# Kernel optimization log

Measured on AMD Instinct MI355X. Metric: run time of the kernel, lower is better.

Reference implementation:

```python
import jax, jax.numpy as jnp
import numpy as np

B, N, C = 4, 2048, 512
H = 8
HD = C // H  # 64
SCALE = HD ** -0.5


def setup_inputs() -> dict:
    key = jax.random.key(0)
    k1, k2, k3 = jax.random.split(key, 3)
    x = jax.random.normal(k1, (B, N, C), dtype=jnp.float32)
    w_qkv = jax.random.normal(k2, (3 * C, C), dtype=jnp.float32) * (C ** -0.5)
    b_qkv = jnp.zeros((3 * C,), dtype=jnp.float32)
    w_proj = jax.random.normal(k3, (C, C), dtype=jnp.float32) * (C ** -0.5)
    b_proj = jnp.zeros((C,), dtype=jnp.float32)
    return {"x": x, "w_qkv": w_qkv, "b_qkv": b_qkv, "w_proj": w_proj, "b_proj": b_proj}


def reference(x, w_qkv, b_qkv, w_proj, b_proj):
    # qkv projection: (B,N,C) @ (C,3C) -> (B,N,3,H,HD) -> (3,B,H,N,HD)
    qkv = (x @ w_qkv.T + b_qkv).reshape(B, N, 3, H, HD).transpose(2, 0, 3, 1, 4)
    q, k, v = qkv[0], qkv[1], qkv[2]
    # scores (B,H,N,N), scale applied after matmul as in the torch source
    attn = jnp.einsum('bhnd,bhmd->bhnm', q, k) * SCALE
    attn = jax.nn.softmax(attn, axis=-1)
    out = jnp.einsum('bhnm,bhmd->bhnd', attn, v)  # (B,H,N,HD)
    out = out.transpose(0, 2, 1, 3).reshape(B, N, C)
    return out @ w_proj.T + b_proj
```

## Files before the change

### kernel.cpp

```cpp
#include <hip/hip_runtime.h>

#define B_ 4
#define N_ 2048
#define C_ 512
#define H_ 8
#define HD_ 64
#define SCALE_ 0.125f
#define QSCALE_ 0.18033688011112042f

typedef __attribute__((ext_vector_type(8))) __bf16 bf16x8;
typedef __attribute__((ext_vector_type(4))) float f32x4;
typedef __attribute__((ext_vector_type(4))) unsigned int u32x4;
typedef __attribute__((ext_vector_type(2))) unsigned int u32x2;
typedef __attribute__((ext_vector_type(4))) short s16x4;

#if __has_builtin(__builtin_amdgcn_mfma_f32_16x16x16bf16_1k)
#define MFMA16(acc, a, b) acc = __builtin_amdgcn_mfma_f32_16x16x16bf16_1k(a, b, acc, 0, 0, 0)
#else
#define MFMA16(acc, a, b) \
    asm("v_mfma_f32_16x16x16_bf16 %0, %1, %2, %0" : "+v"(acc) : "v"(a), "v"(b))
#endif

__device__ __forceinline__ unsigned short f2bf(float f) {
    unsigned int u = __builtin_bit_cast(unsigned int, f);
    u += 0x7fffu + ((u >> 16) & 1u);
    return (unsigned short)(u >> 16);
}

__device__ __forceinline__ void llds16(const void* g, void* l) {
    __builtin_amdgcn_global_load_lds(
        (const __attribute__((address_space(1))) unsigned int*)g,
        (__attribute__((address_space(3))) unsigned int*)l, 16, 0, 0);
}

__global__ __launch_bounds__(256) void cvt_all(const float* __restrict__ x,
                                               const float* __restrict__ wq,
                                               const float* __restrict__ wp,
                                               unsigned short* __restrict__ xb,
                                               unsigned short* __restrict__ wqb,
                                               unsigned short* __restrict__ wpb) {
    const int NX = B_ * N_ * C_ / 4, NQ = 3 * C_ * C_ / 4, NP = C_ * C_ / 4;
    int i = blockIdx.x * 256 + threadIdx.x;
    const float4* src;
    ushort4* dst;
    int idx;
    if (i < NX) { src = (const float4*)x; dst = (ushort4*)xb; idx = i; }
    else if (i < NX + NQ) { src = (const float4*)wq; dst = (ushort4*)wqb; idx = i - NX; }
    else if (i < NX + NQ + NP) { src = (const float4*)wp; dst = (ushort4*)wpb; idx = i - NX - NQ; }
    else return;
    float4 v = src[idx];
    ushort4 o;
    o.x = f2bf(v.x); o.y = f2bf(v.y); o.z = f2bf(v.z); o.w = f2bf(v.w);
    dst[idx] = o;
}

template <int MODE>
__global__ __launch_bounds__(256) void gemm_bt(const unsigned short* __restrict__ A,
                                               const unsigned short* __restrict__ Bw,
                                               const float* __restrict__ bias,
                                               float* __restrict__ Out,
                                               unsigned short* __restrict__ Qb,
                                               unsigned short* __restrict__ Kb,
                                               unsigned short* __restrict__ Vt) {
    constexpr int K = 512;
    __shared__ __align__(16) unsigned char smem[32768];
    unsigned char* sA = smem;
    unsigned char* sB = smem + 16384;

    const int tid = threadIdx.x;
    const int lane = tid & 63;
    const int wave = tid >> 6;
    const int wm = wave >> 1, wn = wave & 1;
    const int m0 = blockIdx.y * 128;
    const int n0 = blockIdx.x * 128;

    f32x4 acc[4][4] = {};

    for (int k0 = 0; k0 < K; k0 += 64) {
#pragma unroll
        for (int i = 0; i < 4; i++) {
            int ci = wave * 4 + i;
            int row = ci * 8 + (lane >> 3);
            int cb = (lane & 7) * 16;
            const unsigned char* ga =
                (const unsigned char*)A + ((size_t)(m0 + row) * K + k0) * 2 + cb;
            const unsigned char* gb =
                (const unsigned char*)Bw + ((size_t)(n0 + row) * K + k0) * 2 + cb;
            llds16(ga, sA + ci * 1024);
            llds16(gb, sB + ci * 1024);
        }
        __syncthreads();
#pragma unroll
        for (int kk = 0; kk < 2; kk++) {
            bf16x8 af[4], bfr[4];
#pragma unroll
            for (int mi = 0; mi < 4; mi++)
                af[mi] = *(const bf16x8*)(sA + (wm * 64 + mi * 16 + (lane & 15)) * 128 +
                                          kk * 64 + (lane >> 4) * 16);
#pragma unroll
            for (int ni = 0; ni < 4; ni++)
                bfr[ni] = *(const bf16x8*)(sB + (wn * 64 + ni * 16 + (lane & 15)) * 128 +
                                           kk * 64 + (lane >> 4) * 16);
#pragma unroll
            for (int mi = 0; mi < 4; mi++)
#pragma unroll
                for (int ni = 0; ni < 4; ni++)
                    acc[mi][ni] = __builtin_amdgcn_mfma_f32_16x16x32_bf16(
                        af[mi], bfr[ni], acc[mi][ni], 0, 0, 0);
        }
        __syncthreads();
    }

    if constexpr (MODE == 0) {
        if (n0 >= 1024) {
            unsigned char* T = smem;
#pragma unroll
            for (int ni = 0; ni < 4; ni++) {
                int cl = wn * 64 + ni * 16 + (lane & 15);
                float bv = bias[n0 + cl];
#pragma unroll
                for (int mi = 0; mi < 4; mi++) {
#pragma unroll
                    for (int r = 0; r < 4; r++) {
                        int ml = wm * 64 + mi * 16 + ((lane >> 4) << 2) + r;
                        *(unsigned short*)(T + cl * 256 + ((ml * 2) ^ ((cl & 7) << 4))) =
                            f2bf(acc[mi][ni][r] + bv);
                    }
                }
            }
            __syncthreads();
            const int b = m0 >> 11;
#pragma unroll
            for (int it = 0; it < 8; it++) {
                int li = it * 256 + tid;
                int cl2 = li >> 4, mc = li & 15;
                int cg = n0 + cl2;
                int h = (cg >> 6) & 7, d = cg & 63;
                u32x4 vv = *(const u32x4*)(T + cl2 * 256 + ((mc * 16) ^ ((cl2 & 7) << 4)));
                int n = (m0 & (N_ - 1)) + mc * 8;
                *(u32x4*)((unsigned char*)Vt +
                          (((size_t)(b * H_ + h) * HD_ + d) * N_ + n) * 2) = vv;
            }
        } else {
            const bool selq = (n0 < 512);
#pragma unroll
            for (int ni = 0; ni < 4; ni++) {
                int cg = n0 + wn * 64 + ni * 16 + (lane & 15);
                int h = (cg >> 6) & 7, d = cg & 63;
                float bv = bias[cg];
#pragma unroll
                for (int mi = 0; mi < 4; mi++) {
#pragma unroll
                    for (int r = 0; r < 4; r++) {
                        int m = m0 + wm * 64 + mi * 16 + ((lane >> 4) << 2) + r;
                        int b = m >> 11, n = m & (N_ - 1);
                        float fv = acc[mi][ni][r] + bv;
                        size_t idx = ((size_t)(b * H_ + h) * N_ + n) * HD_ + d;
                        if (selq) Qb[idx] = f2bf(fv * QSCALE_);
                        else Kb[idx] = f2bf(fv);
                    }
                }
            }
        }
    } else {
#pragma unroll
        for (int ni = 0; ni < 4; ni++) {
            int c = n0 + wn * 64 + ni * 16 + (lane & 15);
            float bv = bias[c];
#pragma unroll
            for (int mi = 0; mi < 4; mi++) {
#pragma unroll
                for (int r = 0; r < 4; r++) {
                    int m = m0 + wm * 64 + mi * 16 + ((lane >> 4) << 2) + r;
                    Out[(size_t)m * C_ + c] = acc[mi][ni][r] + bv;
                }
            }
        }
    }
}

__global__ __launch_bounds__(512, 4) void attn_fwd(const unsigned short* __restrict__ Qb,
                                                   const unsigned short* __restrict__ Kb,
                                                   const unsigned short* __restrict__ Vt,
                                                   unsigned short* __restrict__ AO) {
    __shared__ __align__(16) unsigned char smem[32768];

    const int tid = threadIdx.x, lane = tid & 63, wave = tid >> 6;
    const int g = lane >> 4, c = lane & 15;
    const int L = blockIdx.y * 16 + blockIdx.x;
    const int bh = (L & 7) * 4 + ((L >> 3) & 3);
    const int qx = L >> 5;
    const int q0 = qx * 128 + wave * 16;
    const unsigned short* Qh = Qb + (size_t)bh * N_ * HD_;
    const unsigned short* Kh = Kb + (size_t)bh * N_ * HD_;
    const unsigned short* Vh = Vt + (size_t)bh * HD_ * N_;

    bf16x8 qf[2];
#pragma unroll
    for (int kk = 0; kk < 2; kk++)
        qf[kk] = *(const bf16x8*)(Qh + (size_t)(q0 + c) * HD_ + kk * 32 + g * 8);

    s16x4 ones16;
#pragma unroll
    for (int i = 0; i < 4; i++) ones16[i] = (short)0x3F80;

    f32x4 o[4] = {};
    f32x4 osum = {};

    const int srow = tid >> 3;
    const int sslot = (tid & 7) * 16;
    const int ssw = (sslot ^ ((srow & 7) << 4));

    {
        u32x4 kreg = *(const u32x4*)((const unsigned char*)Kh + (size_t)srow * 128 + sslot);
        u32x4 vreg = *(const u32x4*)((const unsigned char*)Vh + (size_t)srow * (N_ * 2) + sslot);
        *(u32x4*)(smem + srow * 128 + ssw) = kreg;
        *(u32x4*)(smem + 16384 + srow * 128 + ssw) = vreg;
    }
    __syncthreads();

#pragma unroll 1
    for (int t = 0; t < N_ / 64; t++) {
        unsigned char* bK = smem + (t & 1) * 8192;
        unsigned char* bV = smem + 16384 + (t & 1) * 8192;

        u32x4 kreg, vreg;
        if (t < N_ / 64 - 1) {
            int kv0 = (t + 1) * 64;
            kreg = *(const u32x4*)((const unsigned char*)Kh + (size_t)(kv0 + srow) * 128 + sslot);
            vreg = *(const u32x4*)((const unsigned char*)Vh + (size_t)srow * (N_ * 2) +
                                   kv0 * 2 + sslot);
        }

        f32x4 s[4] = {};
#pragma unroll
        for (int j = 0; j < 4; j++) {
#pragma unroll
            for (int kk = 0; kk < 2; kk++) {
                int krow = j * 16 + c;
                bf16x8 kf = *(const bf16x8*)(bK + krow * 128 +
                                             ((kk * 64 + g * 16) ^ ((krow & 7) << 4)));
                s[j] = __builtin_amdgcn_mfma_f32_16x16x32_bf16(kf, qf[kk], s[j], 0, 0, 0);
            }
        }

        s16x4 pa[4];
#pragma unroll
        for (int j = 0; j < 4; j++) {
            float p0 = __builtin_exp2f(s[j][0]);
            float p1 = __builtin_exp2f(s[j][1]);
            float p2 = __builtin_exp2f(s[j][2]);
            float p3 = __builtin_exp2f(s[j][3]);
            unsigned int lo, hi;
            asm("v_cvt_pk_bf16_f32 %0, %1, %2" : "=v"(lo) : "v"(p0), "v"(p1));
            asm("v_cvt_pk_bf16_f32 %0, %1, %2" : "=v"(hi) : "v"(p2), "v"(p3));
            u32x2 w;
            w[0] = lo;
            w[1] = hi;
            pa[j] = __builtin_bit_cast(s16x4, w);
        }

#pragma unroll
        for (int j = 0; j < 4; j++) {
            MFMA16(osum, pa[j], ones16);
#pragma unroll
            for (int dj = 0; dj < 4; dj++) {
                int vrow = dj * 16 + c;
                u32x2 vv = *(const u32x2*)(bV + vrow * 128 +
                                           ((j * 32 + 8 * g) ^ ((vrow & 7) << 4)));
                s16x4 vfj = __builtin_bit_cast(s16x4, vv);
                MFMA16(o[dj], pa[j], vfj);
            }
        }

        if (t < N_ / 64 - 1) {
            unsigned char* nK = smem + ((t + 1) & 1) * 8192;
            unsigned char* nV = smem + 16384 + ((t + 1) & 1) * 8192;
            *(u32x4*)(nK + srow * 128 + ssw) = kreg;
            *(u32x4*)(nV + srow * 128 + ssw) = vreg;
        }
        __syncthreads();
    }

    const int b = bh >> 3, h = bh & 7;
#pragma unroll
    for (int r = 0; r < 4; r++) {
        float inv = 1.0f / osum[r];
        int n = q0 + (g << 2) + r;
#pragma unroll
        for (int dj = 0; dj < 4; dj++) {
            int col = h * HD_ + dj * 16 + c;
            AO[((size_t)(b * N_ + n)) * C_ + col] = f2bf(o[dj][r] * inv);
        }
    }
}

extern "C" void kernel_launch(void* const* d_in, const int* in_sizes, int n_in,
                              void* d_out, int out_size, void* d_ws, size_t ws_size,
                              hipStream_t stream) {
    const float* x = (const float*)d_in[0];
    const float* w_qkv = (const float*)d_in[1];
    const float* b_qkv = (const float*)d_in[2];
    const float* w_proj = (const float*)d_in[3];
    const float* b_proj = (const float*)d_in[4];
    float* out = (float*)d_out;

    unsigned char* ws = (unsigned char*)d_ws;
    unsigned short* xb = (unsigned short*)ws;
    unsigned short* AO = xb;
    unsigned short* wqb = (unsigned short*)(ws + 8388608);
    unsigned short* wpb = (unsigned short*)(ws + 8388608 + 1572864);
    unsigned short* Vt = (unsigned short*)(ws + 8388608 + 1572864 + 524288);

    unsigned short* Qb = (unsigned short*)d_out;
    unsigned short* Kb = Qb + (size_t)B_ * H_ * N_ * HD_;

    const int NALL = (B_ * N_ * C_ + 3 * C_ * C_ + C_ * C_) / 4;
    cvt_all<<<(NALL + 255) / 256, 256, 0, stream>>>(x, w_qkv, w_proj, xb, wqb, wpb);

    gemm_bt<0><<<dim3(12, 64), 256, 0, stream>>>(xb, wqb, b_qkv, nullptr, Qb, Kb, Vt);
    attn_fwd<<<dim3(16, 32), 512, 0, stream>>>(Qb, Kb, Vt, AO);
    gemm_bt<1><<<dim3(4, 64), 256, 0, stream>>>(AO, wpb, b_proj, out, nullptr, nullptr, nullptr);
}
```

Measured before the change: 112.1 us.

## Split attention waves across KV halves with 32-row query tiles and LDS reduction

Each wave now handles 32 query rows and half of each 64-key tile, instead of 16 query rows over the full tile. Each K and V fragment read from LDS feeds two MFMAs, so LDS reads per MFMA drop. The two key-half partial outputs and row sums are combined through shared memory at the end. This costs a larger LDS allocation, more accumulator registers and an extra barrier plus reduction in the epilogue.

```diff
diff --git a/kernel.cpp b/kernel.cpp
--- a/kernel.cpp
+++ b/kernel.cpp
@@ -183,29 +183,33 @@
                                                    const unsigned short* __restrict__ Kb,
                                                    const unsigned short* __restrict__ Vt,
                                                    unsigned short* __restrict__ AO) {
-    __shared__ __align__(16) unsigned char smem[32768];
+    __shared__ __align__(16) unsigned char smem[40960];
 
     const int tid = threadIdx.x, lane = tid & 63, wave = tid >> 6;
     const int g = lane >> 4, c = lane & 15;
+    const int wq = wave >> 1, wk = wave & 1;
     const int L = blockIdx.y * 16 + blockIdx.x;
     const int bh = (L & 7) * 4 + ((L >> 3) & 3);
     const int qx = L >> 5;
-    const int q0 = qx * 128 + wave * 16;
+    const int q0 = qx * 128 + wq * 32;
     const unsigned short* Qh = Qb + (size_t)bh * N_ * HD_;
     const unsigned short* Kh = Kb + (size_t)bh * N_ * HD_;
     const unsigned short* Vh = Vt + (size_t)bh * HD_ * N_;
 
-    bf16x8 qf[2];
-#pragma unroll
-    for (int kk = 0; kk < 2; kk++)
-        qf[kk] = *(const bf16x8*)(Qh + (size_t)(q0 + c) * HD_ + kk * 32 + g * 8);
+    bf16x8 qf[2][2];
+#pragma unroll
+    for (int u = 0; u < 2; u++)
+#pragma unroll
+        for (int kk = 0; kk < 2; kk++)
+            qf[u][kk] = *(const bf16x8*)(Qh + (size_t)(q0 + u * 16 + c) * HD_ +
+                                         kk * 32 + g * 8);
 
     s16x4 ones16;
 #pragma unroll
     for (int i = 0; i < 4; i++) ones16[i] = (short)0x3F80;
 
-    f32x4 o[4] = {};
-    f32x4 osum = {};
+    f32x4 o[2][4] = {};
+    f32x4 osum[2] = {};
 
     const int srow = tid >> 3;
     const int sslot = (tid & 7) * 16;
@@ -232,44 +236,49 @@
                                    kv0 * 2 + sslot);
         }
 
-        f32x4 s[4] = {};
-#pragma unroll
-        for (int j = 0; j < 4; j++) {
+        f32x4 s[2][2] = {};
+#pragma unroll
+        for (int j = 0; j < 2; j++) {
 #pragma unroll
             for (int kk = 0; kk < 2; kk++) {
-                int krow = j * 16 + c;
+                int krow = wk * 32 + j * 16 + c;
                 bf16x8 kf = *(const bf16x8*)(bK + krow * 128 +
                                              ((kk * 64 + g * 16) ^ ((krow & 7) << 4)));
-                s[j] = __builtin_amdgcn_mfma_f32_16x16x32_bf16(kf, qf[kk], s[j], 0, 0, 0);
-            }
-        }
-
-        s16x4 pa[4];
-#pragma unroll
-        for (int j = 0; j < 4; j++) {
-            float p0 = __builtin_exp2f(s[j][0]);
-            float p1 = __builtin_exp2f(s[j][1]);
-            float p2 = __builtin_exp2f(s[j][2]);
-            float p3 = __builtin_exp2f(s[j][3]);
-            unsigned int lo, hi;
-            asm("v_cvt_pk_bf16_f32 %0, %1, %2" : "=v"(lo) : "v"(p0), "v"(p1));
-            asm("v_cvt_pk_bf16_f32 %0, %1, %2" : "=v"(hi) : "v"(p2), "v"(p3));
-            u32x2 w;
-            w[0] = lo;
-            w[1] = hi;
-            pa[j] = __builtin_bit_cast(s16x4, w);
-        }
-
-#pragma unroll
-        for (int j = 0; j < 4; j++) {
-            MFMA16(osum, pa[j], ones16);
+                s[0][j] = __builtin_amdgcn_mfma_f32_16x16x32_bf16(kf, qf[0][kk], s[0][j], 0, 0, 0);
+                s[1][j] = __builtin_amdgcn_mfma_f32_16x16x32_bf16(kf, qf[1][kk], s[1][j], 0, 0, 0);
+            }
+        }
+
+        s16x4 pa[2][2];
+#pragma unroll
+        for (int u = 0; u < 2; u++)
+#pragma unroll
+            for (int j = 0; j < 2; j++) {
+                float p0 = __builtin_exp2f(s[u][j][0]);
+                float p1 = __builtin_exp2f(s[u][j][1]);
+                float p2 = __builtin_exp2f(s[u][j][2]);
+                float p3 = __builtin_exp2f(s[u][j][3]);
+                unsigned int lo, hi;
+                asm("v_cvt_pk_bf16_f32 %0, %1, %2" : "=v"(lo) : "v"(p0), "v"(p1));
+                asm("v_cvt_pk_bf16_f32 %0, %1, %2" : "=v"(hi) : "v"(p2), "v"(p3));
+                u32x2 w;
+                w[0] = lo;
+                w[1] = hi;
+                pa[u][j] = __builtin_bit_cast(s16x4, w);
+            }
+
+#pragma unroll
+        for (int j = 0; j < 2; j++) {
+            MFMA16(osum[0], pa[0][j], ones16);
+            MFMA16(osum[1], pa[1][j], ones16);
 #pragma unroll
             for (int dj = 0; dj < 4; dj++) {
                 int vrow = dj * 16 + c;
                 u32x2 vv = *(const u32x2*)(bV + vrow * 128 +
-                                           ((j * 32 + 8 * g) ^ ((vrow & 7) << 4)));
+                                           ((wk * 64 + j * 32 + 8 * g) ^ ((vrow & 7) << 4)));
                 s16x4 vfj = __builtin_bit_cast(s16x4, vv);
-                MFMA16(o[dj], pa[j], vfj);
+                MFMA16(o[0][dj], pa[0][j], vfj);
+                MFMA16(o[1][dj], pa[1][j], vfj);
             }
         }
 
@@ -282,16 +291,39 @@
         __syncthreads();
     }
 
-    const int b = bh >> 3, h = bh & 7;
-#pragma unroll
-    for (int r = 0; r < 4; r++) {
-        float inv = 1.0f / osum[r];
-        int n = q0 + (g << 2) + r;
-#pragma unroll
-        for (int dj = 0; dj < 4; dj++) {
-            int col = h * HD_ + dj * 16 + c;
-            AO[((size_t)(b * N_ + n)) * C_ + col] = f2bf(o[dj][r] * inv);
-        }
+    unsigned char* cb = smem + ((size_t)(wq * 64 + lane)) * 160;
+    if (wk == 1) {
+#pragma unroll
+        for (int u = 0; u < 2; u++)
+#pragma unroll
+            for (int dj = 0; dj < 4; dj++)
+                *(f32x4*)(cb + (u * 4 + dj) * 16) = o[u][dj];
+        *(f32x4*)(cb + 128) = osum[0];
+        *(f32x4*)(cb + 144) = osum[1];
+    }
+    __syncthreads();
+    if (wk == 0) {
+#pragma unroll
+        for (int u = 0; u < 2; u++)
+#pragma unroll
+            for (int dj = 0; dj < 4; dj++)
+                o[u][dj] += *(const f32x4*)(cb + (u * 4 + dj) * 16);
+        osum[0] += *(const f32x4*)(cb + 128);
+        osum[1] += *(const f32x4*)(cb + 144);
+
+        const int b = bh >> 3, h = bh & 7;
+#pragma unroll
+        for (int u = 0; u < 2; u++)
+#pragma unroll
+            for (int r = 0; r < 4; r++) {
+                float inv = 1.0f / osum[u][r];
+                int n = q0 + u * 16 + (g << 2) + r;
+#pragma unroll
+                for (int dj = 0; dj < 4; dj++) {
+                    int col = h * HD_ + dj * 16 + c;
+                    AO[((size_t)(b * N_ + n)) * C_ + col] = f2bf(o[u][dj][r] * inv);
+                }
+            }
     }
 }
 
```

After: 114.3 us. 2.0% more time.
